# Performance work log

Measured on AMD Instinct MI355X. Metric: run time of the kernel, lower is better.

## Reference

```python
import jax, jax.numpy as jnp
import numpy as np

N_OBJ = 256   # number of RoIs/objects
C = 151       # num_obj_classes (Visual Genome)
H = 512       # hidden_dim == output_dim
T = 3         # time_step


def setup_inputs() -> dict:
    key = jax.random.key(0)
    ks = jax.random.split(key, 12)
    s = jnp.float32(0.02)

    def lin(k, out_dim, in_dim):
        k1, k2 = jax.random.split(k)
        w = jax.random.normal(k1, (out_dim, in_dim), jnp.float32) * s
        b = jax.random.normal(k2, (out_dim,), jnp.float32) * s
        return w, b

    inp = {}
    inp['input_ggnn'] = jax.random.normal(ks[0], (N_OBJ, H), jnp.float32)
    inp['matrix'] = jax.random.uniform(ks[1], (C, C), jnp.float32)
    for i, name in enumerate(['eq3_w', 'eq3_u', 'eq4_w', 'eq4_u', 'eq5_w', 'eq5_u']):
        in_dim = 2 * H if name.endswith('_w') else H
        w, b = lin(ks[2 + i], H, in_dim)
        inp['w_' + name] = w
        inp['b_' + name] = b
    w, b = lin(ks[8], H, 2 * H)
    inp['w_out'], inp['b_out'] = w, b
    w, b = lin(ks[9], C, C * H)
    inp['w_cls'], inp['b_cls'] = w, b
    return inp


def _ggnn_obj(input_ggnn, matrix,
              w_eq3_w, b_eq3_w, w_eq3_u, b_eq3_u,
              w_eq4_w, b_eq4_w, w_eq4_u, b_eq4_u,
              w_eq5_w, b_eq5_w, w_eq5_u, b_eq5_u,
              w_out, b_out, w_cls, b_cls):
    n = input_ggnn.shape[0]
    # hidden[i, c] = input_ggnn[i] for every class slot c  -> [N, C, H]
    hidden0 = jnp.broadcast_to(input_ggnn[:, None, :], (n, C, H))

    def step(hidden, _):
        hidden_sum = hidden.sum(axis=0)                # [C, H]
        x = hidden_sum[None, :, :] - hidden            # [N, C, H]
        # matrix.T @ x_i  and  matrix @ x_i, vectorized over N
        av1 = jnp.einsum('cd,nch->ndh', matrix, x)     # M^T propagation
        av2 = jnp.einsum('dc,nch->ndh', matrix, x)     # M propagation
        av = jnp.concatenate([av1, av2], axis=-1).reshape(n * C, 2 * H)
        h = hidden.reshape(n * C, H)
        zv = jax.nn.sigmoid(av @ w_eq3_w.T + b_eq3_w + h @ w_eq3_u.T + b_eq3_u)
        rv = jax.nn.sigmoid(av @ w_eq4_w.T + b_eq4_w + h @ w_eq4_u.T + b_eq4_u)
        hv = jnp.tanh(av @ w_eq5_w.T + b_eq5_w + (rv * h) @ w_eq5_u.T + b_eq5_u)
        h = (1.0 - zv) * h + zv * hv
        return h.reshape(n, C, H), None

    hidden, _ = jax.lax.scan(step, hidden0, None, length=T)

    inp_rep = hidden0.reshape(n * C, H)                # input repeated per class slot
    out = jnp.concatenate([hidden.reshape(n * C, H), inp_rep], axis=1)  # [N*C, 2H]
    out = jax.nn.relu(out @ w_out.T + b_out)           # [N*C, H]
    obj_dists = out.reshape(n, C * H) @ w_cls.T + b_cls  # [N, C]
    return obj_dists


def reference(input_ggnn, matrix,
              w_eq3_w, b_eq3_w, w_eq3_u, b_eq3_u,
              w_eq4_w, b_eq4_w, w_eq4_u, b_eq4_u,
              w_eq5_w, b_eq5_w, w_eq5_u, b_eq5_u,
              w_out, b_out, w_cls, b_cls):
    return _ggnn_obj(input_ggnn, matrix,
                     w_eq3_w, b_eq3_w, w_eq3_u, b_eq3_u,
                     w_eq4_w, b_eq4_w, w_eq4_u, b_eq4_u,
                     w_eq5_w, b_eq5_w, w_eq5_u, b_eq5_u,
                     w_out, b_out, w_cls, b_cls)
```

## Files before the change

kernel.cpp:

```cpp
#include <hip/hip_runtime.h>


#define C_     151
#define H_     512
#define NOBJ   256
#define NR     38656
#define NCH    64
#define CH     9664
#define CHP    9728
#define KPAD   160
#define KLDS   168
#define KA     2560
#define KV     3584

typedef _Float16 half8 __attribute__((ext_vector_type(8)));
typedef _Float16 half4 __attribute__((ext_vector_type(4)));
typedef float    f32x4 __attribute__((ext_vector_type(4)));

__device__ __forceinline__ float sigm(float x) { return 1.f / (1.f + expf(-x)); }

__device__ __forceinline__ void gload16(const void* g, void* l) {
    __builtin_amdgcn_global_load_lds(
        (const __attribute__((address_space(1))) void*)g,
        (__attribute__((address_space(3))) void*)l, 16, 0, 0);
}

__device__ __forceinline__ int kqswz(int s) {
    return 8 * (((s & 3) + 8 - ((s >> 2) & 3) - ((s >> 4) & 3)) & 3);
}
__device__ __forceinline__ int fraswz(int lane) {
    const int lb = lane & 15;
    return lb * 32 + 8 * (((lane >> 4) + lb + (lb >> 2)) & 3);
}

__device__ __forceinline__ half8 loadA8(const _Float16* p) { return *(const half8*)p; }
__device__ __forceinline__ half8 loadA8(const float* p) {
    f32x4 a = *(const f32x4*)p;
    f32x4 b = *(const f32x4*)(p + 4);
    half8 o;
    #pragma unroll
    for (int j = 0; j < 4; ++j) { o[j] = (_Float16)a[j]; o[4 + j] = (_Float16)b[j]; }
    return o;
}

template<int OP, typename AT, bool DUPK>
__global__ __launch_bounds__(256, 2)
void gemm_kernel(const AT* __restrict__ A, int lda,
                 const _Float16* __restrict__ B, int ldb,
                 void* __restrict__ Out, int ldo,
                 const float* __restrict__ bias,
                 const float* __restrict__ bias2,
                 int kchunk, int chunkStride)
{
    constexpr bool A16 = (sizeof(AT) == 2);
    __shared__ _Float16 sA[128 * 32];
    __shared__ _Float16 sB[128 * 32];
    const int tid  = threadIdx.x;
    const int lane = tid & 63;
    const int w    = tid >> 6;
    const int m0   = blockIdx.x * 128;
    const int n0   = blockIdx.y * 128;
    const int kbase = blockIdx.z * kchunk;

    const int s0 = tid, s1 = tid + 256;
    const AT* Ap0 = A + (size_t)(m0 + (s0 >> 2)) * lda + kqswz(s0);
    const AT* Ap1 = A + (size_t)(m0 + (s1 >> 2)) * lda + kqswz(s1);
    const _Float16* Bp0 = B + (size_t)(n0 + (s0 >> 2)) * ldb + kbase + kqswz(s0);
    const _Float16* Bp1 = B + (size_t)(n0 + (s1 >> 2)) * ldb + kbase + kqswz(s1);
    const int la0 = 8 * s0;
    const int la1 = 8 * s1;
    _Float16* lA0 = &sA[w * 512];
    _Float16* lA1 = &sA[2048 + w * 512];
    _Float16* lB0 = &sB[w * 512];
    _Float16* lB1 = &sB[2048 + w * 512];

    f32x4 acc[4][4];
    #pragma unroll
    for (int i = 0; i < 4; ++i)
        #pragma unroll
        for (int j = 0; j < 4; ++j)
            #pragma unroll
            for (int r = 0; r < 4; ++r) acc[i][j][r] = 0.f;

    const int mrow = (w >> 1) * 64;
    const int ncol = (w & 1) * 64;
    const int fra  = fraswz(lane);

    for (int k0 = 0; k0 < kchunk; k0 += 32) {
        int kA;
        if (DUPK) kA = (k0 < 2048) ? k0 : ((k0 < 3072) ? k0 - 2048 : k0 - 1024);
        else      kA = kbase + k0;
        if constexpr (A16) {
            __syncthreads();
            gload16(Ap0 + kA, lA0);
            gload16(Ap1 + kA, lA1);
            gload16(Bp0 + k0, lB0);
            gload16(Bp1 + k0, lB1);
            __syncthreads();
        } else {
            half8 va0 = loadA8(Ap0 + kA);
            half8 va1 = loadA8(Ap1 + kA);
            half8 vb0 = *(const half8*)(Bp0 + k0);
            half8 vb1 = *(const half8*)(Bp1 + k0);
            __syncthreads();
            *(half8*)&sA[la0] = va0;
            *(half8*)&sA[la1] = va1;
            *(half8*)&sB[la0] = vb0;
            *(half8*)&sB[la1] = vb1;
            __syncthreads();
        }
        half8 af[4], bf[4];
        #pragma unroll
        for (int i = 0; i < 4; ++i)
            af[i] = *(const half8*)&sA[(mrow + i * 16) * 32 + fra];
        #pragma unroll
        for (int i = 0; i < 4; ++i)
            bf[i] = *(const half8*)&sB[(ncol + i * 16) * 32 + fra];
        #pragma unroll
        for (int mi = 0; mi < 4; ++mi)
            #pragma unroll
            for (int ni = 0; ni < 4; ++ni)
                acc[mi][ni] = __builtin_amdgcn_mfma_f32_16x16x32_f16(af[mi], bf[ni], acc[mi][ni], 0, 0, 0);
    }

    const size_t zoff = (size_t)blockIdx.z * (size_t)chunkStride;
    #pragma unroll
    for (int mi = 0; mi < 4; ++mi) {
        #pragma unroll
        for (int ni = 0; ni < 4; ++ni) {
            #pragma unroll
            for (int r = 0; r < 4; ++r) {
                const int row = m0 + mrow + mi * 16 + (lane >> 4) * 4 + r;
                const int col = n0 + ncol + ni * 16 + (lane & 15);
                float v = acc[mi][ni][r];
                const size_t o = zoff + (size_t)row * ldo + col;
                if (OP == 0) {
                    ((float*)Out)[o] = v;
                } else if (OP == 1) {
                    ((_Float16*)Out)[o] = (_Float16)v;
                } else {
                    const unsigned n = (unsigned)row / 151u;
                    v += bias[col] + bias2[n * 512u + col];
                    v = v > 0.f ? v : 0.f;
                    ((_Float16*)Out)[o] = (_Float16)v;
                }
            }
        }
    }
}

template<int OP, bool DUPK>
__global__ __launch_bounds__(512, 2)
void gemm_wide(const _Float16* __restrict__ A, int lda,
               const _Float16* __restrict__ B, int ldb,
               void* __restrict__ Out, int ldo,
               int kchunk, int chunkStride)
{
    __shared__ _Float16 sA[128 * 32];
    __shared__ _Float16 sB[256 * 32];
    const int tid  = threadIdx.x;
    const int lane = tid & 63;
    const int w    = tid >> 6;
    const int m0   = blockIdx.x * 128;
    const int n0   = blockIdx.y * 256;
    const int kbase = blockIdx.z * kchunk;

    const int kq = kqswz(tid);
    const _Float16* Ap = A + (size_t)(m0 + (tid >> 2)) * lda + kq;
    const _Float16* Bp0 = B + (size_t)(n0 + (tid >> 2)) * ldb + kbase + kq;
    const _Float16* Bp1 = B + (size_t)(n0 + 128 + (tid >> 2)) * ldb + kbase + kq;
    _Float16* lA  = &sA[w * 512];
    _Float16* lB0 = &sB[w * 512];
    _Float16* lB1 = &sB[4096 + w * 512];

    f32x4 acc[4][4];
    #pragma unroll
    for (int i = 0; i < 4; ++i)
        #pragma unroll
        for (int j = 0; j < 4; ++j)
            #pragma unroll
            for (int r = 0; r < 4; ++r) acc[i][j][r] = 0.f;

    const int mrow = (w >> 2) * 64;
    const int ncol = (w & 3) * 64;
    const int fra  = fraswz(lane);

    for (int k0 = 0; k0 < kchunk; k0 += 32) {
        int kA;
        if (DUPK) kA = (k0 < 2048) ? k0 : ((k0 < 3072) ? k0 - 2048 : k0 - 1024);
        else      kA = kbase + k0;
        __syncthreads();
        gload16(Ap + kA, lA);
        gload16(Bp0 + k0, lB0);
        gload16(Bp1 + k0, lB1);
        __syncthreads();
        half8 af[4], bf[4];
        #pragma unroll
        for (int i = 0; i < 4; ++i)
            af[i] = *(const half8*)&sA[(mrow + i * 16) * 32 + fra];
        #pragma unroll
        for (int i = 0; i < 4; ++i)
            bf[i] = *(const half8*)&sB[(ncol + i * 16) * 32 + fra];
        #pragma unroll
        for (int mi = 0; mi < 4; ++mi)
            #pragma unroll
            for (int ni = 0; ni < 4; ++ni)
                acc[mi][ni] = __builtin_amdgcn_mfma_f32_16x16x32_f16(af[mi], bf[ni], acc[mi][ni], 0, 0, 0);
    }

    const size_t zoff = (size_t)blockIdx.z * (size_t)chunkStride;
    #pragma unroll
    for (int mi = 0; mi < 4; ++mi) {
        #pragma unroll
        for (int ni = 0; ni < 4; ++ni) {
            #pragma unroll
            for (int r = 0; r < 4; ++r) {
                const int row = m0 + mrow + mi * 16 + (lane >> 4) * 4 + r;
                const int col = n0 + ncol + ni * 16 + (lane & 15);
                const float v = acc[mi][ni][r];
                const size_t o = zoff + (size_t)row * ldo + col;
                if (OP == 0) ((float*)Out)[o] = v;
                else         ((_Float16*)Out)[o] = (_Float16)v;
            }
        }
    }
}

__global__ __launch_bounds__(256, 2)
void mix_kernel(const float* __restrict__ hid, const float* __restrict__ S,
                const _Float16* __restrict__ MTh, const _Float16* __restrict__ MTl,
                const _Float16* __restrict__ Mrh, const _Float16* __restrict__ Mrl,
                _Float16* __restrict__ AVH, int cbase)
{
    __shared__ _Float16 sxh[64 * KLDS];
    __shared__ _Float16 sxl[64 * KLDS];
    const int n  = blockIdx.x;
    const int h0 = blockIdx.y * 64;
    const int tid = threadIdx.x;

    #pragma unroll
    for (int i = 0; i < 5; ++i) {
        const int s  = tid + 256 * i;
        const int c  = s >> 3;
        const int hg = s & 7;
        half8 oh, ol;
        if (c < C_) {
            const float* hp = &hid[(size_t)(cbase + n * C_ + c) * H_ + h0 + hg * 8];
            const float* sp = &S[c * H_ + h0 + hg * 8];
            half8 hh;
            #pragma unroll
            for (int j = 0; j < 8; ++j) {
                const float hv = hp[j];
                const float x = sp[j] - hv;
                const _Float16 hi = (_Float16)x;
                oh[j] = hi;
                ol[j] = (_Float16)(x - (float)hi);
                hh[j] = (_Float16)hv;
            }
            *(half8*)&AVH[(size_t)(n * C_ + c) * KA + 2048 + h0 + hg * 8] = hh;
        } else {
            #pragma unroll
            for (int j = 0; j < 8; ++j) { oh[j] = (_Float16)0.f; ol[j] = (_Float16)0.f; }
        }
        #pragma unroll
        for (int j = 0; j < 8; ++j) {
            sxh[(hg * 8 + j) * KLDS + c] = oh[j];
            sxl[(hg * 8 + j) * KLDS + c] = ol[j];
        }
    }
    __syncthreads();

    const int lane = tid & 63;
    const int w    = tid >> 6;
    const _Float16* Mhi = (w >> 1) ? Mrh : MTh;
    const _Float16* Mlo = (w >> 1) ? Mrl : MTl;
    const int hb = (w & 1) * 32;

    f32x4 acc[10][2];
    #pragma unroll
    for (int i = 0; i < 10; ++i)
        #pragma unroll
        for (int j = 0; j < 2; ++j)
            #pragma unroll
            for (int r = 0; r < 4; ++r) acc[i][j][r] = 0.f;

    #pragma unroll
    for (int pass = 0; pass < 3; ++pass) {
        const _Float16* Ma = (pass == 2) ? Mlo : Mhi;
        const _Float16* X  = (pass == 1) ? sxl : sxh;
        #pragma unroll
        for (int kk = 0; kk < 5; ++kk) {
            const int k0 = kk * 32;
            half8 bf[2];
            #pragma unroll
            for (int ht = 0; ht < 2; ++ht)
                bf[ht] = *(const half8*)&X[(hb + ht * 16 + (lane & 15)) * KLDS + k0 + 8 * (lane >> 4)];
            #pragma unroll
            for (int dt = 0; dt < 10; ++dt) {
                half8 af = *(const half8*)&Ma[(dt * 16 + (lane & 15)) * KPAD + k0 + 8 * (lane >> 4)];
                acc[dt][0] = __builtin_amdgcn_mfma_f32_16x16x32_f16(af, bf[0], acc[dt][0], 0, 0, 0);
                acc[dt][1] = __builtin_amdgcn_mfma_f32_16x16x32_f16(af, bf[1], acc[dt][1], 0, 0, 0);
            }
        }
    }

    const int mixoff = (w >> 1) * 512;
    #pragma unroll
    for (int dt = 0; dt < 10; ++dt) {
        #pragma unroll
        for (int ht = 0; ht < 2; ++ht) {
            #pragma unroll
            for (int r = 0; r < 4; ++r) {
                const int d = dt * 16 + (lane >> 4) * 4 + r;
                if (d < C_) {
                    const int h = h0 + hb + ht * 16 + (lane & 15);
                    const float v = acc[dt][ht][r];
                    const _Float16 hi = (_Float16)v;
                    const _Float16 lo = (_Float16)(v - (float)hi);
                    _Float16* rowp = AVH + (size_t)(n * C_ + d) * KA + mixoff + h;
                    rowp[0]    = hi;
                    rowp[1024] = lo;
                }
            }
        }
    }
}


__global__ void k_sreduce(const float* __restrict__ hid, float* __restrict__ Stmp)
{
    const int c  = blockIdx.x;
    const int g  = blockIdx.y;
    const int hw = threadIdx.x;
    const float* p = hid + (size_t)c * H_ + hw * 8;
    float s[8];
    #pragma unroll
    for (int j = 0; j < 8; ++j) s[j] = 0.f;
    const size_t stride = (size_t)C_ * H_;
    for (int n = g * 32; n < g * 32 + 32; ++n) {
        f32x4 a = *(const f32x4*)(p + (size_t)n * stride);
        f32x4 b = *(const f32x4*)(p + (size_t)n * stride + 4);
        #pragma unroll
        for (int j = 0; j < 4; ++j) { s[j] += a[j]; s[4 + j] += b[j]; }
    }
    float* o = Stmp + (size_t)g * (C_ * H_) + c * H_ + hw * 8;
    *(f32x4*)o       = f32x4{s[0], s[1], s[2], s[3]};
    *(f32x4*)(o + 4) = f32x4{s[4], s[5], s[6], s[7]};
}

__global__ void k_sfold(const float* __restrict__ Stmp, float* __restrict__ S)
{
    const int idx = blockIdx.x * 256 + threadIdx.x;
    float s = 0.f;
    #pragma unroll
    for (int g = 0; g < 8; ++g) s += Stmp[(size_t)g * (C_ * H_) + idx];
    S[idx] = s;
}

__global__ void k_ew1(_Float16* __restrict__ pre, const float* __restrict__ hid,
                      const float* __restrict__ bz, const float* __restrict__ br, int cbase)
{
    const int idx = blockIdx.x * 256 + threadIdx.x;
    const unsigned r = idx >> 7;
    const int o4 = (idx & 127) << 2;
    const size_t base = (size_t)r * 1536;
    half4 zp = *(const half4*)&pre[base + o4];
    half4 rp = *(const half4*)&pre[base + 512 + o4];
    f32x4 hd = *(const f32x4*)&hid[(size_t)(cbase + r) * H_ + o4];
    f32x4 bz4 = *(const f32x4*)&bz[o4];
    f32x4 br4 = *(const f32x4*)&br[o4];
    half4 zs, rh;
    #pragma unroll
    for (int j = 0; j < 4; ++j) {
        float z = sigm((float)zp[j] + bz4[j]);
        float rr = sigm((float)rp[j] + br4[j]);
        zs[j] = (_Float16)z;
        rh[j] = (_Float16)(rr * hd[j]);
    }
    *(half4*)&pre[base + o4] = zs;
    *(half4*)&pre[base + 512 + o4] = rh;
}

__global__ void k_ew2(const _Float16* __restrict__ pre, const _Float16* __restrict__ p5a,
                      const _Float16* __restrict__ p5b,
                      float* __restrict__ hid, const float* __restrict__ b5, int cbase)
{
    const int idx = blockIdx.x * 256 + threadIdx.x;
    const unsigned r = idx >> 7;
    const int o4 = (idx & 127) << 2;
    const size_t base = (size_t)r * 1536;
    half4 w5 = *(const half4*)&pre[base + 1024 + o4];
    half4 pa = *(const half4*)&p5a[(size_t)r * H_ + o4];
    half4 pb = *(const half4*)&p5b[(size_t)r * H_ + o4];
    half4 zz = *(const half4*)&pre[base + o4];
    f32x4 hd = *(const f32x4*)&hid[(size_t)(cbase + r) * H_ + o4];
    f32x4 b54 = *(const f32x4*)&b5[o4];
    #pragma unroll
    for (int j = 0; j < 4; ++j) {
        float t = tanhf((float)w5[j] + (float)pa[j] + (float)pb[j] + b54[j]);
        float z = (float)zz[j];
        hd[j] = (1.f - z) * hd[j] + z * t;
    }
    *(f32x4*)&hid[(size_t)(cbase + r) * H_ + o4] = hd;
}


__global__ void prep_wbig(const float* w3w, const float* w3u,
                          const float* w4w, const float* w4u,
                          const float* w5w, const float* w5u,
                          _Float16* __restrict__ Wbig)
{
    const int idx = blockIdx.x * 256 + threadIdx.x;
    const int op = idx / KV;
    const int j = idx - op * KV;
    const int g = op >> 9, o = op & 511;
    const float* ww = (g == 0) ? w3w : (g == 1) ? w4w : w5w;
    const float* wu = (g == 0) ? w3u : (g == 1) ? w4u : w5u;
    _Float16 out;
    if (j < 1024) {
        out = (_Float16)ww[o * 1024 + j];
    } else if (j < 2048) {
        out = (_Float16)ww[o * 1024 + (j - 1024)];
    } else if (j < 3072) {
        const float v = ww[o * 1024 + (j - 2048)];
        const _Float16 hi = (_Float16)v;
        out = (_Float16)(v - (float)hi);
    } else {
        out = (g < 2) ? (_Float16)wu[o * 512 + (j - 3072)] : (_Float16)0.f;
    }
    Wbig[idx] = out;
}

__global__ void prep_m(const float* __restrict__ matrix,
                       _Float16* __restrict__ MTh, _Float16* __restrict__ MTl,
                       _Float16* __restrict__ Mrh, _Float16* __restrict__ Mrl)
{
    const int idx = blockIdx.x * 256 + threadIdx.x;
    const int d = idx / KPAD, c = idx - d * KPAD;
    float vT = 0.f, vR = 0.f;
    if (d < C_ && c < C_) { vT = matrix[c * C_ + d]; vR = matrix[d * C_ + c]; }
    const _Float16 th = (_Float16)vT;
    const _Float16 rh = (_Float16)vR;
    MTh[idx] = th; MTl[idx] = (_Float16)(vT - (float)th);
    Mrh[idx] = rh; Mrl[idx] = (_Float16)(vR - (float)rh);
}

__global__ void prep_wout(const float* __restrict__ wout,
                          _Float16* __restrict__ WL, _Float16* __restrict__ WR)
{
    const int idx = blockIdx.x * 256 + threadIdx.x;
    const int o = idx >> 9, j = idx & 511;
    WL[idx] = (_Float16)wout[o * 1024 + j];
    WR[idx] = (_Float16)wout[o * 1024 + 512 + j];
}

__global__ void prep_wcls(const float* __restrict__ wcls, _Float16* __restrict__ w16)
{
    const int k = blockIdx.x * 256 + threadIdx.x;
    const int d = blockIdx.y;
    _Float16 v = (_Float16)0.f;
    if (d < C_) v = (_Float16)wcls[(size_t)d * (C_ * H_) + k];
    w16[(size_t)d * (C_ * H_) + k] = v;
}

__global__ void k_cast(const float* __restrict__ src, _Float16* __restrict__ dst, int n)
{
    const int i = blockIdx.x * 256 + threadIdx.x;
    if (i < n) dst[i] = (_Float16)src[i];
}

__global__ void prep_bias(const float* b3w, const float* b3u, const float* b4w,
                          const float* b4u, const float* b5w, const float* b5u,
                          float* bz, float* br, float* b5)
{
    const int i = threadIdx.x;
    bz[i] = b3w[i] + b3u[i];
    br[i] = b4w[i] + b4u[i];
    b5[i] = b5w[i] + b5u[i];
}

__global__ void prep_hid(const float* __restrict__ input, float* __restrict__ hid)
{
    const int idx = blockIdx.x * 256 + threadIdx.x;
    const unsigned row = idx >> 7;
    const int h4 = (idx & 127) << 2;
    const unsigned n = row / 151u;
    f32x4 v = *(const f32x4*)&input[(size_t)n * H_ + h4];
    *(f32x4*)&hid[(size_t)row * H_ + h4] = v;
}

__global__ void k_reduce(const float* __restrict__ partial, const float* __restrict__ bcls,
                         float* __restrict__ out)
{
    const int idx = blockIdx.x * 256 + threadIdx.x;
    const unsigned n = (unsigned)idx / 151u;
    const unsigned d = (unsigned)idx - n * 151u;
    float s = 0.f;
    for (int z = 0; z < C_; ++z)
        s += partial[(size_t)z * (NOBJ * 256) + n * 256 + d];
    out[idx] = s + bcls[d];
}


extern "C" void kernel_launch(void* const* d_in, const int* in_sizes, int n_in,
                              void* d_out, int out_size, void* d_ws, size_t ws_size,
                              hipStream_t stream)
{
    const float* input  = (const float*)d_in[0];
    const float* matrix = (const float*)d_in[1];
    const float* w3w = (const float*)d_in[2];
    const float* b3w = (const float*)d_in[3];
    const float* w3u = (const float*)d_in[4];
    const float* b3u = (const float*)d_in[5];
    const float* w4w = (const float*)d_in[6];
    const float* b4w = (const float*)d_in[7];
    const float* w4u = (const float*)d_in[8];
    const float* b4u = (const float*)d_in[9];
    const float* w5w = (const float*)d_in[10];
    const float* b5w = (const float*)d_in[11];
    const float* w5u = (const float*)d_in[12];
    const float* b5u = (const float*)d_in[13];
    const float* wout = (const float*)d_in[14];
    const float* bout = (const float*)d_in[15];
    const float* wcls = (const float*)d_in[16];
    const float* bcls = (const float*)d_in[17];
    float* obj = (float*)d_out;

    char* ws = (char*)d_ws;
    size_t off = 0;
    auto take = [&](size_t bytes) -> char* {
        off = (off + 255) & ~(size_t)255;
        char* p = ws + off;
        off += bytes;
        return p;
    };

    _Float16* Wbig  = (_Float16*)take((size_t)1536 * KV * 2);
    _Float16* MTh   = (_Float16*)take((size_t)KPAD * KPAD * 2);
    _Float16* MTl   = (_Float16*)take((size_t)KPAD * KPAD * 2);
    _Float16* Mrh   = (_Float16*)take((size_t)KPAD * KPAD * 2);
    _Float16* Mrl   = (_Float16*)take((size_t)KPAD * KPAD * 2);
    _Float16* W5u16 = (_Float16*)take((size_t)512 * 512 * 2);
    _Float16* WL16  = (_Float16*)take((size_t)512 * 512 * 2);
    _Float16* WR16  = (_Float16*)take((size_t)512 * 512 * 2);
    _Float16* in16  = (_Float16*)take((size_t)256 * 512 * 2);
    float*    bz    = (float*)take(512 * 4);
    float*    br    = (float*)take(512 * 4);
    float*    b5    = (float*)take(512 * 4);
    float*    Stmp  = (float*)take((size_t)8 * C_ * H_ * 4);
    float*    S32   = (float*)take((size_t)C_ * H_ * 4);
    float*    base  = (float*)take((size_t)256 * 512 * 4);
    float*    hid32 = (float*)take((size_t)NR * H_ * 4);
    _Float16* AVH   = (_Float16*)take((size_t)CHP * KA * 2);
    _Float16* prec  = (_Float16*)take((size_t)CHP * 1536 * 2);
    _Float16* p5u = AVH;
    _Float16* OUT16 = AVH;
    _Float16* Wcls16 = (_Float16*)hid32;
    float* partial = (float*)((char*)hid32 + (size_t)NOBJ * C_ * H_ * 2);

    (void)in_sizes; (void)n_in; (void)out_size; (void)ws_size;

    prep_wbig<<<dim3((1536 * KV) / 256), 256, 0, stream>>>(w3w, w3u, w4w, w4u, w5w, w5u, Wbig);
    prep_m<<<dim3((KPAD * KPAD) / 256), 256, 0, stream>>>(matrix, MTh, MTl, Mrh, Mrl);
    k_cast<<<dim3((512 * 512) / 256), 256, 0, stream>>>(w5u, W5u16, 512 * 512);
    prep_wout<<<dim3((512 * 512) / 256), 256, 0, stream>>>(wout, WL16, WR16);
    k_cast<<<dim3((256 * 512) / 256), 256, 0, stream>>>(input, in16, 256 * 512);
    prep_bias<<<dim3(1), 512, 0, stream>>>(b3w, b3u, b4w, b4u, b5w, b5u, bz, br, b5);
    prep_hid<<<dim3((NR * 128) / 256), 256, 0, stream>>>(input, hid32);
    gemm_kernel<0, _Float16, false><<<dim3(2, 4, 1), 256, 0, stream>>>(
        in16, 512, WR16, 512, base, 512, nullptr, nullptr, 512, 0);

    for (int t = 0; t < 3; ++t) {
        k_sreduce<<<dim3(C_, 8), 64, 0, stream>>>(hid32, Stmp);
        k_sfold<<<dim3((C_ * H_) / 256), 256, 0, stream>>>(Stmp, S32);
        for (int cc = 0; cc < 4; ++cc) {
            const int cbase = cc * CH;
            mix_kernel<<<dim3(NCH, 8), 256, 0, stream>>>(
                hid32, S32, MTh, MTl, Mrh, Mrl, AVH, cbase);
            gemm_wide<1, true><<<dim3(CHP / 128, 1536 / 256, 1), 512, 0, stream>>>(
                AVH, KA, Wbig, KV, prec, 1536, KV, 0);
            k_ew1<<<dim3((CH * 128) / 256), 256, 0, stream>>>(prec, hid32, bz, br, cbase);
            gemm_kernel<1, _Float16, false><<<dim3(CHP / 128, 4, 2), 256, 0, stream>>>(
                prec + 512, 1536, W5u16, 512, p5u, 512, nullptr, nullptr, 256, CHP * 512);
            k_ew2<<<dim3((CH * 128) / 256), 256, 0, stream>>>(
                prec, p5u, p5u + (size_t)CHP * 512, hid32, b5, cbase);
        }
    }

    gemm_kernel<2, float, false><<<dim3(NR / 128, 512 / 128, 1), 256, 0, stream>>>(
        hid32, 512, WL16, 512, OUT16, 512, bout, base, 512, 0);

    prep_wcls<<<dim3((C_ * H_) / 256, 256), 256, 0, stream>>>(wcls, Wcls16);
    gemm_kernel<0, _Float16, false><<<dim3(NOBJ / 128, 256 / 128, C_), 256, 0, stream>>>(
        OUT16, C_ * H_, Wcls16, C_ * H_, partial, 256, nullptr, nullptr, 512, NOBJ * 256);
    k_reduce<<<dim3(NR / 256), 256, 0, stream>>>(partial, bcls, obj);
}
```

Measured before the change: 2.777 ms.

## Fuse GRU gate elementwise ops into GEMM epilogues and drop split-K

Folds the sigmoid gates and the r*h product into the epilogue of the wide gate GEMM, and folds the tanh plus hidden-state update into the epilogue of the W5u GEMM. This removes two elementwise kernels and their round trips of the pre-activation buffers. The W5u GEMM also goes from a 2-way split-K with partial outputs to a single pass over the full K. The cost is heavier epilogues with scattered, uncoalesced global loads, and fewer blocks in the second GEMM.

Measured after the change: 3.213 ms. 1.16x slower.

```diff
diff --git a/kernel.cpp b/kernel.cpp
--- a/kernel.cpp
+++ b/kernel.cpp
@@ -50,7 +50,9 @@
                  void* __restrict__ Out, int ldo,
                  const float* __restrict__ bias,
                  const float* __restrict__ bias2,
-                 int kchunk, int chunkStride)
+                 int kchunk, int chunkStride,
+                 const _Float16* __restrict__ X1,
+                 float* __restrict__ hidp, int cbase)
 {
     constexpr bool A16 = (sizeof(AT) == 2);
     __shared__ _Float16 sA[128 * 32];
@@ -138,11 +140,20 @@
                     ((float*)Out)[o] = v;
                 } else if (OP == 1) {
                     ((_Float16*)Out)[o] = (_Float16)v;
-                } else {
+                } else if (OP == 2) {
                     const unsigned n = (unsigned)row / 151u;
                     v += bias[col] + bias2[n * 512u + col];
                     v = v > 0.f ? v : 0.f;
                     ((_Float16*)Out)[o] = (_Float16)v;
+                } else {
+                    if (row < CH) {
+                        const size_t pb = (size_t)row * 1536;
+                        const float w5 = (float)X1[pb + 1024 + col];
+                        const float zv = (float)X1[pb + col];
+                        const float t  = tanhf(v + w5 + bias[col]);
+                        float* hp = &hidp[(size_t)(cbase + row) * H_ + col];
+                        *hp = (1.f - zv) * (*hp) + zv * t;
+                    }
                 }
             }
         }
@@ -154,7 +165,10 @@
 void gemm_wide(const _Float16* __restrict__ A, int lda,
                const _Float16* __restrict__ B, int ldb,
                void* __restrict__ Out, int ldo,
-               int kchunk, int chunkStride)
+               int kchunk, int chunkStride,
+               const float* __restrict__ bz,
+               const float* __restrict__ br,
+               const float* __restrict__ hidp, int cbase)
 {
     __shared__ _Float16 sA[128 * 32];
     __shared__ _Float16 sB[256 * 32];
@@ -217,10 +231,21 @@
             for (int r = 0; r < 4; ++r) {
                 const int row = m0 + mrow + mi * 16 + (lane >> 4) * 4 + r;
                 const int col = n0 + ncol + ni * 16 + (lane & 15);
-                const float v = acc[mi][ni][r];
+                float v = acc[mi][ni][r];
                 const size_t o = zoff + (size_t)row * ldo + col;
-                if (OP == 0) ((float*)Out)[o] = v;
-                else         ((_Float16*)Out)[o] = (_Float16)v;
+                if (OP == 3) {
+                    if (col < 512) {
+                        v = sigm(v + bz[col]);
+                    } else if (col < 1024) {
+                        const float rr = sigm(v + br[col - 512]);
+                        const float h = (row < CH)
+                            ? hidp[(size_t)(cbase + row) * H_ + (col - 512)] : 0.f;
+                        v = rr * h;
+                    }
+                    ((_Float16*)Out)[o] = (_Float16)v;
+                } else {
+                    ((_Float16*)Out)[o] = (_Float16)v;
+                }
             }
         }
     }
@@ -355,53 +380,6 @@
     #pragma unroll
     for (int g = 0; g < 8; ++g) s += Stmp[(size_t)g * (C_ * H_) + idx];
     S[idx] = s;
-}
-
-__global__ void k_ew1(_Float16* __restrict__ pre, const float* __restrict__ hid,
-                      const float* __restrict__ bz, const float* __restrict__ br, int cbase)
-{
-    const int idx = blockIdx.x * 256 + threadIdx.x;
-    const unsigned r = idx >> 7;
-    const int o4 = (idx & 127) << 2;
-    const size_t base = (size_t)r * 1536;
-    half4 zp = *(const half4*)&pre[base + o4];
-    half4 rp = *(const half4*)&pre[base + 512 + o4];
-    f32x4 hd = *(const f32x4*)&hid[(size_t)(cbase + r) * H_ + o4];
-    f32x4 bz4 = *(const f32x4*)&bz[o4];
-    f32x4 br4 = *(const f32x4*)&br[o4];
-    half4 zs, rh;
-    #pragma unroll
-    for (int j = 0; j < 4; ++j) {
-        float z = sigm((float)zp[j] + bz4[j]);
-        float rr = sigm((float)rp[j] + br4[j]);
-        zs[j] = (_Float16)z;
-        rh[j] = (_Float16)(rr * hd[j]);
-    }
-    *(half4*)&pre[base + o4] = zs;
-    *(half4*)&pre[base + 512 + o4] = rh;
-}
-
-__global__ void k_ew2(const _Float16* __restrict__ pre, const _Float16* __restrict__ p5a,
-                      const _Float16* __restrict__ p5b,
-                      float* __restrict__ hid, const float* __restrict__ b5, int cbase)
-{
-    const int idx = blockIdx.x * 256 + threadIdx.x;
-    const unsigned r = idx >> 7;
-    const int o4 = (idx & 127) << 2;
-    const size_t base = (size_t)r * 1536;
-    half4 w5 = *(const half4*)&pre[base + 1024 + o4];
-    half4 pa = *(const half4*)&p5a[(size_t)r * H_ + o4];
-    half4 pb = *(const half4*)&p5b[(size_t)r * H_ + o4];
-    half4 zz = *(const half4*)&pre[base + o4];
-    f32x4 hd = *(const f32x4*)&hid[(size_t)(cbase + r) * H_ + o4];
-    f32x4 b54 = *(const f32x4*)&b5[o4];
-    #pragma unroll
-    for (int j = 0; j < 4; ++j) {
-        float t = tanhf((float)w5[j] + (float)pa[j] + (float)pb[j] + b54[j]);
-        float z = (float)zz[j];
-        hd[j] = (1.f - z) * hd[j] + z * t;
-    }
-    *(f32x4*)&hid[(size_t)(cbase + r) * H_ + o4] = hd;
 }
 
 
@@ -553,7 +531,6 @@
     float*    hid32 = (float*)take((size_t)NR * H_ * 4);
     _Float16* AVH   = (_Float16*)take((size_t)CHP * KA * 2);
     _Float16* prec  = (_Float16*)take((size_t)CHP * 1536 * 2);
-    _Float16* p5u = AVH;
     _Float16* OUT16 = AVH;
     _Float16* Wcls16 = (_Float16*)hid32;
     float* partial = (float*)((char*)hid32 + (size_t)NOBJ * C_ * H_ * 2);
@@ -568,7 +545,7 @@
     prep_bias<<<dim3(1), 512, 0, stream>>>(b3w, b3u, b4w, b4u, b5w, b5u, bz, br, b5);
     prep_hid<<<dim3((NR * 128) / 256), 256, 0, stream>>>(input, hid32);
     gemm_kernel<0, _Float16, false><<<dim3(2, 4, 1), 256, 0, stream>>>(
-        in16, 512, WR16, 512, base, 512, nullptr, nullptr, 512, 0);
+        in16, 512, WR16, 512, base, 512, nullptr, nullptr, 512, 0, nullptr, nullptr, 0);
 
     for (int t = 0; t < 3; ++t) {
         k_sreduce<<<dim3(C_, 8), 64, 0, stream>>>(hid32, Stmp);
@@ -577,21 +554,20 @@
             const int cbase = cc * CH;
             mix_kernel<<<dim3(NCH, 8), 256, 0, stream>>>(
                 hid32, S32, MTh, MTl, Mrh, Mrl, AVH, cbase);
-            gemm_wide<1, true><<<dim3(CHP / 128, 1536 / 256, 1), 512, 0, stream>>>(
-                AVH, KA, Wbig, KV, prec, 1536, KV, 0);
-            k_ew1<<<dim3((CH * 128) / 256), 256, 0, stream>>>(prec, hid32, bz, br, cbase);
-            gemm_kernel<1, _Float16, false><<<dim3(CHP / 128, 4, 2), 256, 0, stream>>>(
-                prec + 512, 1536, W5u16, 512, p5u, 512, nullptr, nullptr, 256, CHP * 512);
-            k_ew2<<<dim3((CH * 128) / 256), 256, 0, stream>>>(
-                prec, p5u, p5u + (size_t)CHP * 512, hid32, b5, cbase);
+            gemm_wide<3, true><<<dim3(CHP / 128, 1536 / 256, 1), 512, 0, stream>>>(
+                AVH, KA, Wbig, KV, prec, 1536, KV, 0, bz, br, hid32, cbase);
+            gemm_kernel<3, _Float16, false><<<dim3(CHP / 128, 4, 1), 256, 0, stream>>>(
+                prec + 512, 1536, W5u16, 512, nullptr, 512, b5, nullptr, 512, 0,
+                prec, hid32, cbase);
         }
     }
 
     gemm_kernel<2, float, false><<<dim3(NR / 128, 512 / 128, 1), 256, 0, stream>>>(
-        hid32, 512, WL16, 512, OUT16, 512, bout, base, 512, 0);
+        hid32, 512, WL16, 512, OUT16, 512, bout, base, 512, 0, nullptr, nullptr, 0);
 
     prep_wcls<<<dim3((C_ * H_) / 256, 256), 256, 0, stream>>>(wcls, Wcls16);
     gemm_kernel<0, _Float16, false><<<dim3(NOBJ / 128, 256 / 128, C_), 256, 0, stream>>>(
-        OUT16, C_ * H_, Wcls16, C_ * H_, partial, 256, nullptr, nullptr, 512, NOBJ * 256);
+        OUT16, C_ * H_, Wcls16, C_ * H_, partial, 256, nullptr, nullptr, 512, NOBJ * 256,
+        nullptr, nullptr, 0);
     k_reduce<<<dim3(NR / 256), 256, 0, stream>>>(partial, bcls, obj);
 }
```

## Switch wide GEMM to 32x32x16 MFMA and trim classifier weight prep

Applied to the files above, without the earlier changes.

The main wide GEMM kernel now uses 32x32x16 f16 MFMA instructions with 2x2 tiles of 16-wide accumulators per wave instead of 4x4 tiles of 16x16x32 MFMAs. LDS fragment offsets are recomputed to match the new operand layout, and the store epilogue is rewritten. The aim is fewer MFMA issues and LDS reads per k-step. Separately, prep_wcls now launches only C_ rows instead of 256 and drops the zero-fill branch, so padded rows 151..255 of the classifier weight buffer are no longer written and depend on whatever that buffer already holds.

After: 2.862 ms. 1.03x slower.

```diff
diff --git a/kernel.cpp b/kernel.cpp
--- a/kernel.cpp
+++ b/kernel.cpp
@@ -16,6 +16,7 @@
 typedef _Float16 half8 __attribute__((ext_vector_type(8)));
 typedef _Float16 half4 __attribute__((ext_vector_type(4)));
 typedef float    f32x4 __attribute__((ext_vector_type(4)));
+typedef float    f32x16 __attribute__((ext_vector_type(16)));
 
 __device__ __forceinline__ float sigm(float x) { return 1.f / (1.f + expf(-x)); }
 
@@ -173,17 +174,22 @@
     _Float16* lB0 = &sB[w * 512];
     _Float16* lB1 = &sB[4096 + w * 512];
 
-    f32x4 acc[4][4];
-    #pragma unroll
-    for (int i = 0; i < 4; ++i)
-        #pragma unroll
-        for (int j = 0; j < 4; ++j)
-            #pragma unroll
-            for (int r = 0; r < 4; ++r) acc[i][j][r] = 0.f;
+    f32x16 acc[2][2];
+    #pragma unroll
+    for (int i = 0; i < 2; ++i)
+        #pragma unroll
+        for (int j = 0; j < 2; ++j)
+            #pragma unroll
+            for (int r = 0; r < 16; ++r) acc[i][j][r] = 0.f;
 
     const int mrow = (w >> 2) * 64;
     const int ncol = (w & 3) * 64;
-    const int fra  = fraswz(lane);
+    const int l31  = lane & 31;
+    const int khi  = lane >> 5;
+    int poff[2];
+    #pragma unroll
+    for (int q = 0; q < 2; ++q)
+        poff[q] = 8 * (((2 * q + khi) + (l31 & 3) + ((l31 >> 2) & 3)) & 3);
 
     for (int k0 = 0; k0 < kchunk; k0 += 32) {
         int kA;
@@ -194,33 +200,41 @@
         gload16(Bp0 + k0, lB0);
         gload16(Bp1 + k0, lB1);
         __syncthreads();
-        half8 af[4], bf[4];
-        #pragma unroll
-        for (int i = 0; i < 4; ++i)
-            af[i] = *(const half8*)&sA[(mrow + i * 16) * 32 + fra];
-        #pragma unroll
-        for (int i = 0; i < 4; ++i)
-            bf[i] = *(const half8*)&sB[(ncol + i * 16) * 32 + fra];
-        #pragma unroll
-        for (int mi = 0; mi < 4; ++mi)
-            #pragma unroll
-            for (int ni = 0; ni < 4; ++ni)
-                acc[mi][ni] = __builtin_amdgcn_mfma_f32_16x16x32_f16(af[mi], bf[ni], acc[mi][ni], 0, 0, 0);
+        half8 af[2][2], bf[2][2];
+        #pragma unroll
+        for (int q = 0; q < 2; ++q) {
+            #pragma unroll
+            for (int mi = 0; mi < 2; ++mi)
+                af[q][mi] = *(const half8*)&sA[(mrow + mi * 32 + l31) * 32 + poff[q]];
+            #pragma unroll
+            for (int ni = 0; ni < 2; ++ni)
+                bf[q][ni] = *(const half8*)&sB[(ncol + ni * 32 + l31) * 32 + poff[q]];
+        }
+        #pragma unroll
+        for (int mi = 0; mi < 2; ++mi)
+            #pragma unroll
+            for (int ni = 0; ni < 2; ++ni) {
+                acc[mi][ni] = __builtin_amdgcn_mfma_f32_32x32x16_f16(af[0][mi], bf[0][ni], acc[mi][ni], 0, 0, 0);
+                acc[mi][ni] = __builtin_amdgcn_mfma_f32_32x32x16_f16(af[1][mi], bf[1][ni], acc[mi][ni], 0, 0, 0);
+            }
     }
 
     const size_t zoff = (size_t)blockIdx.z * (size_t)chunkStride;
     #pragma unroll
-    for (int mi = 0; mi < 4; ++mi) {
-        #pragma unroll
-        for (int ni = 0; ni < 4; ++ni) {
-            #pragma unroll
-            for (int r = 0; r < 4; ++r) {
-                const int row = m0 + mrow + mi * 16 + (lane >> 4) * 4 + r;
-                const int col = n0 + ncol + ni * 16 + (lane & 15);
-                const float v = acc[mi][ni][r];
-                const size_t o = zoff + (size_t)row * ldo + col;
-                if (OP == 0) ((float*)Out)[o] = v;
-                else         ((_Float16*)Out)[o] = (_Float16)v;
+    for (int mi = 0; mi < 2; ++mi) {
+        #pragma unroll
+        for (int ni = 0; ni < 2; ++ni) {
+            #pragma unroll
+            for (int rv = 0; rv < 4; ++rv) {
+                #pragma unroll
+                for (int ri = 0; ri < 4; ++ri) {
+                    const int row = m0 + mrow + mi * 32 + ri + 8 * rv + 4 * khi;
+                    const int col = n0 + ncol + ni * 32 + l31;
+                    const float v = acc[mi][ni][rv * 4 + ri];
+                    const size_t o = zoff + (size_t)row * ldo + col;
+                    if (OP == 0) ((float*)Out)[o] = v;
+                    else         ((_Float16*)Out)[o] = (_Float16)v;
+                }
             }
         }
     }
@@ -458,9 +472,7 @@
 {
     const int k = blockIdx.x * 256 + threadIdx.x;
     const int d = blockIdx.y;
-    _Float16 v = (_Float16)0.f;
-    if (d < C_) v = (_Float16)wcls[(size_t)d * (C_ * H_) + k];
-    w16[(size_t)d * (C_ * H_) + k] = v;
+    w16[(size_t)d * (C_ * H_) + k] = (_Float16)wcls[(size_t)d * (C_ * H_) + k];
 }
 
 __global__ void k_cast(const float* __restrict__ src, _Float16* __restrict__ dst, int n)
@@ -590,7 +602,7 @@
     gemm_kernel<2, float, false><<<dim3(NR / 128, 512 / 128, 1), 256, 0, stream>>>(
         hid32, 512, WL16, 512, OUT16, 512, bout, base, 512, 0);
 
-    prep_wcls<<<dim3((C_ * H_) / 256, 256), 256, 0, stream>>>(wcls, Wcls16);
+    prep_wcls<<<dim3((C_ * H_) / 256, C_), 256, 0, stream>>>(wcls, Wcls16);
     gemm_kernel<0, _Float16, false><<<dim3(NOBJ / 128, 256 / 128, C_), 256, 0, stream>>>(
         OUT16, C_ * H_, Wcls16, C_ * H_, partial, 256, nullptr, nullptr, 512, NOBJ * 256);
     k_reduce<<<dim3(NR / 256), 256, 0, stream>>>(partial, bcls, obj);
```
